# Kernel tuning notes

Hardware: AMD Instinct MI355X
Metric: run time of the kernel (lower is better)

## Reference

```python
import jax, jax.numpy as jnp
import numpy as np

B, C, T, N = 8, 128, 12, 4096
E_HALF = 131072
EPS = 1e-5


def _linear_params(key, fan_in, fan_out):
    kw, kb = jax.random.split(key)
    bound = 1.0 / np.sqrt(fan_in)
    W = jax.random.uniform(kw, (fan_in, fan_out), jnp.float32, -bound, bound)
    b = jax.random.uniform(kb, (fan_out,), jnp.float32, -bound, bound)
    return W, b


def setup_inputs() -> dict:
    key = jax.random.key(0)
    ks = jax.random.split(key, 10)
    h_in = jax.random.normal(ks[0], (B, C, T, N), jnp.float32)
    # symmetric edge list: random pairs + reverses + self loops
    u = jax.random.randint(ks[1], (E_HALF,), 0, N, jnp.int32)
    v = jax.random.randint(ks[2], (E_HALF,), 0, N, jnp.int32)
    loops = jnp.arange(N, dtype=jnp.int32)
    row = jnp.concatenate([u, v, loops])
    col = jnp.concatenate([v, u, loops])
    edge_index = jnp.stack([row, col])  # [2, E]
    Wq, bq = _linear_params(ks[3], C, C)
    Wk, bk = _linear_params(ks[4], C, C)
    Wv, bv = _linear_params(ks[5], C, C)
    W1, b1 = _linear_params(ks[6], 2 * C, 4 * C)
    W2, b2 = _linear_params(ks[7], 4 * C, C)
    W3, b3 = _linear_params(ks[8], C, 1)
    return dict(h_in=h_in, edge_index=edge_index, Wq=Wq, bq=bq, Wk=Wk, bk=bk,
                Wv=Wv, bv=bv, W1=W1, b1=b1, W2=W2, b2=b2, W3=W3, b3=b3)


def _masked_instance_norm(x, mask_f):
    # stats over the non-self-loop edges only (matching torch, where the MLP
    # only sees edge_index[:, non_self_loop_mask])
    cnt = mask_f.sum()
    mean = (x * mask_f).sum(0) / cnt
    var = (((x - mean) ** 2) * mask_f).sum(0) / cnt
    return (x - mean) / jnp.sqrt(var + EPS)


def _forward(h_in, edge_index, Wq, bq, Wk, bk, Wv, bv, W1, b1, W2, b2, W3, b3):
    # ---- TemporalAttention ----
    x = jnp.transpose(h_in, (0, 3, 2, 1))  # [B, N, T, C]
    q = x @ Wq + bq
    k = x @ Wk + bk
    v = x @ Wv + bv
    scores = jnp.einsum('bntc,bnsc->bnts', q, k) / (C ** 0.5)
    attn = jax.nn.softmax(scores, axis=-1)
    weighted = jnp.einsum('bnts,bnsc->bntc', attn, v)
    emb = weighted.sum(axis=2)          # [B, N, C]
    emb_mean = emb.mean(axis=0)         # [N, C]

    # ---- ExtractorMLP on non-self-loop edges ----
    row, col = edge_index[0], edge_index[1]
    self_loop = row == col
    mask_f = (~self_loop).astype(emb_mean.dtype)[:, None]  # [E, 1]
    f12 = jnp.concatenate([emb_mean[row], emb_mean[col]], axis=-1)  # [E, 2C]
    h = jax.nn.relu(_masked_instance_norm(f12 @ W1 + b1, mask_f))
    h = jax.nn.relu(_masked_instance_norm(h @ W2 + b2, mask_f))
    logits = h @ W3 + b3                 # [E, 1]

    # concrete_sample, eval mode (deterministic)
    att = jax.nn.sigmoid(logits)
    all_att = jnp.where(self_loop[:, None], 1.0, att)  # [E, 1]

    # ---- transpose + reorder_like: match each edge with its reverse ----
    M = jnp.max(edge_index) + 1
    fwd_key = row * M + col
    rev_key = col * M + row
    order = jnp.argsort(fwd_key)
    pos = jnp.searchsorted(fwd_key[order], rev_key)
    perm = order[pos]                    # index of reverse edge
    edge_att = (all_att + all_att[perm]) * 0.5
    return edge_att


def reference(h_in, edge_index, Wq, bq, Wk, bk, Wv, bv, W1, b1, W2, b2, W3, b3):
    return _forward(h_in, edge_index, Wq, bq, Wk, bk, Wv, bv, W1, b1, W2, b2, W3, b3)
```

## Files before the change

kernel.cpp:

```cpp
#include <hip/hip_runtime.h>
#include <hip/hip_bf16.h>

#define CC     128
#define TT     12
#define NNODE  4096
#define NE     266240
#define EHALF  131072
#define F1     512
#define EPS    1e-5f
#define RSQRTC 0.08838834764831845f
#define LOG2E  1.4426950408889634f
#define EBG    48
#define NBLKG2 5547
#define NF2B   87
#define ST     40

#define O_XWM   0ull
#define O_ICNT  524288ull
#define O_CNT   524416ull
#define O_T     528512ull
#define O_S     528640ull
#define O_T2    545024ull
#define O_GTB   561664ull
#define O_W0B   569856ull
#define O_WC1   569920ull
#define O_WC2   635456ull
#define O_B1C   700992ull
#define O_M1    701504ull
#define O_IS1   702016ull
#define O_M2    702528ull
#define O_AW    702656ull
#define O_W2T   702784ull
#define O_PB    735552ull
#define O_QB    1784128ull
#define O_ALLA  2832704ull
#define O_PART  3098944ull
#define O_PART2 4518976ull
#define O_Z2    4541248ull

typedef __attribute__((ext_vector_type(8))) short bf16x8;
typedef __attribute__((ext_vector_type(4))) float f32x4;

__device__ inline float bfbits2f(unsigned int v) { return __uint_as_float(v << 16); }
__device__ inline unsigned short f2bf(float x) {
  union { __hip_bfloat16 h; unsigned short u; } cv;
  cv.h = __float2bfloat16(x);
  return cv.u;
}
__device__ inline float f4get(const float4& v, int k) {
  return k == 0 ? v.x : k == 1 ? v.y : k == 2 ? v.z : v.w;
}

__global__ __launch_bounds__(256) void k_setup(
    const float* __restrict__ Wq, const float* __restrict__ bq,
    const float* __restrict__ Wk, const float* __restrict__ Wv,
    const float* __restrict__ bv, const float* __restrict__ W1,
    const float* __restrict__ b1, const float* __restrict__ W2,
    const int* __restrict__ row, const int* __restrict__ col,
    unsigned short* __restrict__ Gtb, unsigned short* __restrict__ w0b,
    float* __restrict__ Wc1, float* __restrict__ Wc2, float* __restrict__ b1c,
    unsigned short* __restrict__ W2T, int* __restrict__ cnt, int* __restrict__ icnt) {
  __shared__ float wvr[CC];
  __shared__ int h[NNODE];
  const int blk = blockIdx.x, tid = threadIdx.x;
  if (blk < 128) {
    if (tid < 128) {
      int i = blk, j = tid;
      float acc = 0.f;
      for (int co = 0; co < CC; ++co) acc = fmaf(Wq[i*CC+co], Wk[j*CC+co], acc);
      Gtb[j*CC + i] = f2bf(acc);
      if (j == 0) {
        float a = 0.f;
        for (int co = 0; co < CC; ++co) a = fmaf(Wk[i*CC+co], bq[co], a);
        w0b[i] = f2bf(a);
      }
    }
  } else if (blk < 256) {
    const int c = blk - 128;
    if (tid < CC) wvr[tid] = Wv[(size_t)c*CC + tid];
    __syncthreads();
    for (int hh = 0; hh < 2; ++hh) {
      int f = hh*256 + tid;
      float a1 = 0.f, a2 = 0.f;
      for (int j = 0; j < CC; ++j) {
        float wv = wvr[j];
        a1 = fmaf(wv, W1[(size_t)j*F1 + f], a1);
        a2 = fmaf(wv, W1[(size_t)(CC + j)*F1 + f], a2);
      }
      Wc1[(size_t)c*F1 + f] = a1;
      Wc2[(size_t)c*F1 + f] = a2;
    }
    if (c == 0) {
      for (int hh = 0; hh < 2; ++hh) {
        int f = hh*256 + tid;
        float s = b1[f];
        for (int j = 0; j < CC; ++j)
          s = fmaf(12.f*bv[j], W1[(size_t)j*F1 + f] + W1[(size_t)(CC + j)*F1 + f], s);
        b1c[f] = s;
      }
    }
  } else if (blk < 384) {
    const int n = blk - 256;
    for (int k = tid; k < F1; k += 256)
      W2T[(size_t)n*F1 + k] = f2bf(W2[(size_t)k*CC + n]);
  } else {
    for (int i = tid; i < NNODE; i += 256) h[i] = 0;
    __syncthreads();
    int lc = 0;
    const int base = (blk - 384) << 12;
    for (int i = tid; i < 4096; i += 256) {
      int e = base + i;
      int r = row[e], c = col[e];
      if (r != c) { atomicAdd(&h[r], 1); ++lc; }
    }
    #pragma unroll
    for (int d = 1; d < 64; d <<= 1) lc += __shfl_xor(lc, d);
    __syncthreads();
    for (int i = tid; i < NNODE; i += 256) { int v = h[i]; if (v) atomicAdd(&cnt[i], v); }
    if ((tid & 63) == 0) atomicAdd(icnt, lc);
  }
}

__global__ __launch_bounds__(256, 8) void k_attn(
    const float* __restrict__ h_in,
    const unsigned short* __restrict__ Gtb,
    const unsigned short* __restrict__ w0b,
    float* __restrict__ xwm) {
  __shared__ unsigned short xs[48*128];
  __shared__ unsigned short ys[49*128];
  const int tid = threadIdx.x;
  const int bid = ((blockIdx.x & 7) << 10) | (blockIdx.x >> 3);
  const int b  = bid >> 10;
  const int n0 = (bid & 1023) << 2;

  const int w = tid >> 6, lane = tid & 63;
  const int l15 = lane & 15, l4 = lane >> 4;

  {
    const int c2 = tid & 63;
    const float* g0 = h_in + (((size_t)b*CC + 2*c2)*TT + w)*NNODE + n0;
    float4 av[3], bv[3];
    #pragma unroll
    for (int it = 0; it < 3; ++it) {
      av[it] = *(const float4*)(g0 + (size_t)(4*it)*NNODE);
      bv[it] = *(const float4*)(g0 + (size_t)(TT + 4*it)*NNODE);
    }
    if (tid < 16) {
      uint4 wv = *(const uint4*)(w0b + (tid << 3));
      *(uint4*)((char*)ys + 48*256 + (tid << 4)) = wv;
    }
    #pragma unroll
    for (int it = 0; it < 3; ++it) {
      int t = w + it*4;
      #pragma unroll
      for (int i = 0; i < 4; ++i) {
        float xa = f4get(av[it], i);
        float xb = f4get(bv[it], i);
        int r = i*TT + t;
        unsigned byte = ((unsigned)r << 8) + (((unsigned)(c2*4)) ^ (((unsigned)(r & 7)) << 4));
        *(unsigned*)((char*)xs + byte) = (unsigned)f2bf(xa) | ((unsigned)f2bf(xb) << 16);
      }
    }
  }
  __syncthreads();

  {
    f32x4 acc[2][3];
    #pragma unroll
    for (int mt = 0; mt < 2; ++mt)
      #pragma unroll
      for (int nt = 0; nt < 3; ++nt) acc[mt][nt] = (f32x4){0.f,0.f,0.f,0.f};

    #pragma unroll
    for (int kt = 0; kt < 4; ++kt) {
      bf16x8 gf[2];
      #pragma unroll
      for (int mt = 0; mt < 2; ++mt)
        gf[mt] = *(const bf16x8*)(Gtb + (size_t)((w<<5) + (mt<<4) + l15)*CC + (kt<<5) + (l4<<3));
      bf16x8 bfr[3];
      #pragma unroll
      for (int nt = 0; nt < 3; ++nt) {
        int rr = nt*16 + l15;
        unsigned byte = ((unsigned)rr << 8) +
                        (((unsigned)((kt<<6) + (l4<<4))) ^ (((unsigned)(rr & 7)) << 4));
        bfr[nt] = *(const bf16x8*)((const char*)xs + byte);
      }
      #pragma unroll
      for (int mt = 0; mt < 2; ++mt)
        #pragma unroll
        for (int nt = 0; nt < 3; ++nt)
          acc[mt][nt] = __builtin_amdgcn_mfma_f32_16x16x32_bf16(gf[mt], bfr[nt], acc[mt][nt], 0, 0, 0);
    }
    #pragma unroll
    for (int mt = 0; mt < 2; ++mt)
      #pragma unroll
      for (int nt = 0; nt < 3; ++nt) {
        int rr = nt*16 + l15;
        ushort4 v;
        v.x = f2bf(acc[mt][nt][0]); v.y = f2bf(acc[mt][nt][1]);
        v.z = f2bf(acc[mt][nt][2]); v.w = f2bf(acc[mt][nt][3]);
        unsigned cb = (unsigned)((w<<6) + (mt<<5) + (l4<<3));
        unsigned byte = ((unsigned)rr << 8) + (cb ^ (((unsigned)(rr & 7)) << 4));
        *(ushort4*)((char*)ys + byte) = v;
      }
  }
  __syncthreads();

  {
    const int rb = w*TT;
    const bool sval = (l15 < TT);
    const int rr  = rb + (sval ? l15 : 0);
    const int rra = sval ? (rb + l15) : 48;
    f32x4 sa = (f32x4){0.f,0.f,0.f,0.f};
    #pragma unroll
    for (int kt = 0; kt < 4; ++kt) {
      unsigned kb = (unsigned)((kt<<6) + (l4<<4));
      unsigned byteA = ((unsigned)rra << 8) + (kb ^ (((unsigned)(rra & 7)) << 4));
      unsigned byteB = ((unsigned)rr  << 8) + (kb ^ (((unsigned)(rr  & 7)) << 4));
      bf16x8 afr = *(const bf16x8*)((const char*)ys + byteA);
      bf16x8 bfr = *(const bf16x8*)((const char*)xs + byteB);
      sa = __builtin_amdgcn_mfma_f32_16x16x32_bf16(afr, bfr, sa, 0, 0, 0);
    }
    float dv = __shfl(sa[0], 48 + l15);
    float p[4];
    #pragma unroll
    for (int r = 0; r < 4; ++r) {
      float t1 = sval ? (sa[r] + dv) * RSQRTC : -1e30f;
      float e = exp2f(t1 * LOG2E);
      float s = e;
      s += __shfl_xor(s, 1);
      s += __shfl_xor(s, 2);
      s += __shfl_xor(s, 4);
      s += __shfl_xor(s, 8);
      p[r] = e / s;
    }
    float wpart = (l4 < 3) ? (p[0] + p[1] + p[2] + p[3]) : 0.f;
    wpart += __shfl_xor(wpart, 16);
    wpart += __shfl_xor(wpart, 32);
    float xw0 = 0.f, xw1 = 0.f;
    #pragma unroll
    for (int s = 0; s < TT; ++s) {
      float wv = __shfl(wpart, s);
      int r2 = rb + s;
      unsigned byte = ((unsigned)r2 << 8) +
                      (((unsigned)(lane << 2)) ^ (((unsigned)(r2 & 7)) << 4));
      unsigned xp = *(const unsigned*)((const char*)xs + byte);
      xw0 = fmaf(wv, bfbits2f(xp & 0xffffu), xw0);
      xw1 = fmaf(wv, bfbits2f(xp >> 16), xw1);
    }
    unsafeAtomicAdd(&xwm[(size_t)(n0 + w)*CC + (lane << 1)],     xw0 * 0.125f);
    unsafeAtomicAdd(&xwm[(size_t)(n0 + w)*CC + (lane << 1) + 1], xw1 * 0.125f);
  }
}

__global__ __launch_bounds__(256) void k_ST2(const float* __restrict__ xwm,
    const int* __restrict__ row, const int* __restrict__ col,
    const int* __restrict__ cnt, float* __restrict__ S,
    float* __restrict__ T2, float* __restrict__ t) {
  __shared__ unsigned short XT[128*ST];
  __shared__ unsigned short YT[128*ST];
  __shared__ float tl[128];
  const int tid = threadIdx.x;
  const int w = tid >> 6, lane = tid & 63, l15 = lane & 15, l4 = lane >> 4;
  const int j = tid & 31, fi = tid >> 5;
  const int f0 = fi << 4;
  f32x4 acc[2][8];
  #pragma unroll
  for (int mt = 0; mt < 2; ++mt)
    #pragma unroll
    for (int nt = 0; nt < 8; ++nt) acc[mt][nt] = (f32x4){0.f,0.f,0.f,0.f};

  if (blockIdx.x < 512) {
    const int ebase = blockIdx.x << 9;
    for (int bt = 0; bt < 16; ++bt) {
      const int e = ebase + (bt << 5) + j;
      const int r = row[e], c = col[e];
      const bool msk = (r != c);
      const float* xr = xwm + (size_t)r*CC + f0;
      const float* xc = xwm + (size_t)c*CC + f0;
      float4 xv[4], yv[4];
      #pragma unroll
      for (int u = 0; u < 4; ++u) { xv[u] = *(const float4*)(xr + 4*u); yv[u] = *(const float4*)(xc + 4*u); }
      __syncthreads();
      #pragma unroll
      for (int u = 0; u < 16; ++u) {
        float xvv = f4get(xv[u >> 2], u & 3);
        float yvv = f4get(yv[u >> 2], u & 3);
        XT[(f0+u)*ST + j] = f2bf(xvv);
        YT[(f0+u)*ST + j] = msk ? f2bf(yvv) : (unsigned short)0;
      }
      __syncthreads();
      bf16x8 af[2];
      #pragma unroll
      for (int mt = 0; mt < 2; ++mt)
        af[mt] = *(const bf16x8*)&XT[((((w<<1)+mt)<<4) + l15)*ST + (l4<<3)];
      #pragma unroll
      for (int nt = 0; nt < 8; ++nt) {
        bf16x8 bf_ = *(const bf16x8*)&YT[(((nt<<4) + l15))*ST + (l4<<3)];
        acc[0][nt] = __builtin_amdgcn_mfma_f32_16x16x32_bf16(af[0], bf_, acc[0][nt], 0, 0, 0);
        acc[1][nt] = __builtin_amdgcn_mfma_f32_16x16x32_bf16(af[1], bf_, acc[1][nt], 0, 0, 0);
      }
    }
    #pragma unroll
    for (int mt = 0; mt < 2; ++mt)
      #pragma unroll
      for (int nt = 0; nt < 8; ++nt)
        #pragma unroll
        for (int reg = 0; reg < 4; ++reg) {
          int a = (((w<<1)+mt)<<4) + (l4<<2) + reg;
          int b = (nt<<4) + l15;
          unsafeAtomicAdd(&S[a*128 + b], acc[mt][nt][reg]);
        }
  } else {
    if (tid < 128) tl[tid] = 0.f;
    float tloc[16];
    #pragma unroll
    for (int u = 0; u < 16; ++u) tloc[u] = 0.f;
    const int nbase = (blockIdx.x - 512) << 7;
    for (int bt = 0; bt < 4; ++bt) {
      const int n = nbase + (bt << 5) + j;
      const float cw = (float)cnt[n];
      const float* xr = xwm + (size_t)n*CC + f0;
      float4 xv[4];
      #pragma unroll
      for (int u = 0; u < 4; ++u) xv[u] = *(const float4*)(xr + 4*u);
      __syncthreads();
      #pragma unroll
      for (int u = 0; u < 16; ++u) {
        float xvv = f4get(xv[u >> 2], u & 3);
        float yvv = cw * xvv;
        XT[(f0+u)*ST + j] = f2bf(xvv);
        YT[(f0+u)*ST + j] = f2bf(yvv);
        tloc[u] += yvv;
      }
      __syncthreads();
      bf16x8 af[2];
      #pragma unroll
      for (int mt = 0; mt < 2; ++mt)
        af[mt] = *(const bf16x8*)&XT[((((w<<1)+mt)<<4) + l15)*ST + (l4<<3)];
      #pragma unroll
      for (int nt = 0; nt < 8; ++nt) {
        bf16x8 bf_ = *(const bf16x8*)&YT[(((nt<<4) + l15))*ST + (l4<<3)];
        acc[0][nt] = __builtin_amdgcn_mfma_f32_16x16x32_bf16(af[0], bf_, acc[0][nt], 0, 0, 0);
        acc[1][nt] = __builtin_amdgcn_mfma_f32_16x16x32_bf16(af[1], bf_, acc[1][nt], 0, 0, 0);
      }
    }
    #pragma unroll
    for (int u = 0; u < 16; ++u) atomicAdd(&tl[f0 + u], tloc[u]);
    #pragma unroll
    for (int mt = 0; mt < 2; ++mt)
      #pragma unroll
      for (int nt = 0; nt < 8; ++nt)
        #pragma unroll
        for (int reg = 0; reg < 4; ++reg) {
          int a = (((w<<1)+mt)<<4) + (l4<<2) + reg;
          int b = (nt<<4) + l15;
          unsafeAtomicAdd(&T2[a*128 + b], acc[mt][nt][reg]);
        }
    __syncthreads();
    if (tid < 128) unsafeAtomicAdd(&t[tid], tl[tid]);
  }
}

__global__ __launch_bounds__(128) void k_stats(const float* __restrict__ S,
    const float* __restrict__ T2, const float* __restrict__ Wc1,
    const float* __restrict__ Wc2, const float* __restrict__ b1c,
    const float* __restrict__ t, const int* __restrict__ icnt,
    float* __restrict__ m1, float* __restrict__ is1) {
  __shared__ float w1c[128], w2c[128];
  __shared__ float redq[2], redt1[2], redt2[2];
  const int f = blockIdx.x, a = threadIdx.x;
  w1c[a] = Wc1[(size_t)a*F1 + f];
  w2c[a] = Wc2[(size_t)a*F1 + f];
  __syncthreads();
  float v1 = 0.f, v2 = 0.f, v3 = 0.f;
  const float* Sr = S + a*128;
  const float* Tr = T2 + a*128;
  for (int b = 0; b < 128; b += 4) {
    float4 sv = *(const float4*)(Sr + b);
    float4 tv = *(const float4*)(Tr + b);
    float4 w1v = *(const float4*)&w1c[b];
    float4 w2v = *(const float4*)&w2c[b];
    #pragma unroll
    for (int u = 0; u < 4; ++u) {
      v1 = fmaf(f4get(sv, u), f4get(w2v, u), v1);
      v2 = fmaf(f4get(tv, u), f4get(w1v, u), v2);
      v3 = fmaf(f4get(tv, u), f4get(w2v, u), v3);
    }
  }
  float pa  = w1c[a]*(v2 + 2.f*v1) + w2c[a]*v3;
  float ta1 = t[a]*w1c[a];
  float ta2 = t[a]*w2c[a];
  #pragma unroll
  for (int d = 1; d < 64; d <<= 1) {
    pa  += __shfl_xor(pa, d);
    ta1 += __shfl_xor(ta1, d);
    ta2 += __shfl_xor(ta2, d);
  }
  if ((a & 63) == 0) { redq[a>>6] = pa; redt1[a>>6] = ta1; redt2[a>>6] = ta2; }
  __syncthreads();
  if (a == 0) {
    float cntf = (float)(*icnt);
    float bb = b1c[f];
    float sumq = redq[0] + redq[1];
    float st1 = redt1[0] + redt1[1];
    float st2 = redt2[0] + redt2[1];
    float w2tot = sumq + 2.f*bb*(st1 + st2) + cntf*bb*bb;
    float w1tot = st1 + st2 + cntf*bb;
    float m = w1tot / cntf;
    m1[f] = m;
    is1[f] = rsqrtf(w2tot/cntf - m*m + EPS);
  }
}

__global__ __launch_bounds__(256) void k_pq(const float* __restrict__ xwm,
    const float* __restrict__ Wc1, const float* __restrict__ Wc2,
    const float* __restrict__ b1c, const float* __restrict__ m1,
    const float* __restrict__ is1,
    unsigned short* __restrict__ Pb, unsigned short* __restrict__ Qb) {
  __shared__ float em[4][CC];
  const int tid = threadIdx.x;
  const int n0 = blockIdx.x << 2;
  for (int i = tid; i < 4*CC; i += 256)
    em[i >> 7][i & 127] = xwm[(size_t)(n0 + (i >> 7))*CC + (i & 127)];
  __syncthreads();
  for (int half = 0; half < 2; ++half) {
    const int f = half*256 + tid;
    const float mm = m1[f], ii = is1[f], bb = b1c[f];
    for (int nn = 0; nn < 4; ++nn) {
      float ap = bb, aq = 0.f;
      for (int c = 0; c < CC; ++c) {
        float e = em[nn][c];
        ap = fmaf(e, Wc1[(size_t)c*F1 + f], ap);
        aq = fmaf(e, Wc2[(size_t)c*F1 + f], aq);
      }
      Pb[(size_t)(n0+nn)*F1 + f] = f2bf(ap * ii);
      Qb[(size_t)(n0+nn)*F1 + f] = f2bf((aq - mm) * ii);
    }
  }
}

__global__ __launch_bounds__(512, 6) void k_gemm(const unsigned short* __restrict__ Pb,
    const unsigned short* __restrict__ Qb, const int* __restrict__ row,
    const int* __restrict__ col,
    const unsigned short* __restrict__ W2T, const float* __restrict__ b2,
    unsigned short* __restrict__ z2, float* __restrict__ part) {
  __shared__ unsigned short h1s[EBG*F1];
  __shared__ int rS[EBG], cS[EBG]; __shared__ float mk[EBG];
  __shared__ float cstat[256];
  const int tid = threadIdx.x;
  const int bid = blockIdx.x;
  const int e0 = bid * EBG;
  const int w = tid >> 6, lane = tid & 63;
  const int wn0 = w << 4;
  const int l15 = lane & 15, l4 = lane >> 4;
  if (tid < EBG) {
    int e = e0 + tid;
    bool valid = e < NE;
    int r = valid ? row[e] : 0, c = valid ? col[e] : 0;
    rS[tid] = r; cS[tid] = c; mk[tid] = (valid && r != c) ? 1.f : 0.f;
  }
  __syncthreads();

  #pragma unroll
  for (int rr = 0; rr < 2; ++rr) {
    int jj[3], cc[3];
    #pragma unroll
    for (int s = 0; s < 3; ++s) {
      int i = tid + ((rr*3 + s) << 9);
      jj[s] = i >> 6; cc[s] = i & 63;
    }
    uint4 pv[3], qv[3];
    #pragma unroll
    for (int s = 0; s < 3; ++s) pv[s] = *(const uint4*)(Pb + (size_t)rS[jj[s]]*F1 + (cc[s] << 3));
    #pragma unroll
    for (int s = 0; s < 3; ++s) qv[s] = *(const uint4*)(Qb + (size_t)cS[jj[s]]*F1 + (cc[s] << 3));
    #pragma unroll
    for (int s = 0; s < 3; ++s) {
      unsigned out[4];
      #pragma unroll
      for (int q = 0; q < 4; ++q) {
        unsigned pu = (&pv[s].x)[q], qu = (&qv[s].x)[q];
        float ha = fmaxf(bfbits2f(pu & 0xffffu) + bfbits2f(qu & 0xffffu), 0.f);
        float hb = fmaxf(bfbits2f(pu >> 16)     + bfbits2f(qu >> 16),     0.f);
        out[q] = (unsigned)f2bf(ha) | ((unsigned)f2bf(hb) << 16);
      }
      unsigned byte = ((unsigned)jj[s] << 10) +
                      (((unsigned)(cc[s] << 4)) ^ (((unsigned)(jj[s] & 7)) << 4));
      *(uint4*)((char*)h1s + byte) = make_uint4(out[0], out[1], out[2], out[3]);
    }
  }
  __syncthreads();

  f32x4 acc[3];
  #pragma unroll
  for (int a = 0; a < 3; ++a) acc[a] = (f32x4){0.f,0.f,0.f,0.f};

  const unsigned short* w2p = W2T + (size_t)(wn0 + l15)*F1 + (l4 << 3);
  #pragma unroll
  for (int kt = 0; kt < 16; ++kt) {
    bf16x8 bfr = *(const bf16x8*)(w2p + (kt << 5));
    bf16x8 afr[3];
    #pragma unroll
    for (int mt = 0; mt < 3; ++mt) {
      int j = (mt << 4) + l15;
      unsigned byte = ((unsigned)j << 10) + (((unsigned)(kt*64 + l4*16)) ^ ((j & 7) << 4));
      afr[mt] = *(const bf16x8*)((const char*)h1s + byte);
    }
    #pragma unroll
    for (int mt = 0; mt < 3; ++mt)
      acc[mt] = __builtin_amdgcn_mfma_f32_16x16x32_bf16(afr[mt], bfr, acc[mt], 0, 0, 0);
  }
  __syncthreads();

  float* z2s = (float*)&h1s[0];
  const int colg = wn0 + l15;
  {
    float bb = b2[colg];
    float sloc = 0.f, qloc = 0.f;
    #pragma unroll
    for (int mt = 0; mt < 3; ++mt) {
      f32x4 v = acc[mt];
      #pragma unroll
      for (int reg = 0; reg < 4; ++reg) {
        int j = (mt << 4) + (l4 << 2) + reg;
        float z = v[reg] + bb;
        float m = mk[j];
        sloc = fmaf(m, z, sloc);
        qloc = fmaf(m*z, z, qloc);
        z2s[j*132 + colg] = z;
      }
    }
    sloc += __shfl_xor(sloc, 16); sloc += __shfl_xor(sloc, 32);
    qloc += __shfl_xor(qloc, 16); qloc += __shfl_xor(qloc, 32);
    if (l4 == 0) { cstat[colg] = sloc; cstat[128 + colg] = qloc; }
  }
  __syncthreads();

  #pragma unroll
  for (int p = 0; p < 2; ++p) {
    int idx = (p << 12) + (tid << 3);
    if (idx < EBG*CC) {
      int j = idx >> 7, c = idx & 127;
      if (e0 + j < NE) {
        const float* src = &z2s[j*132 + c];
        float4 v0 = *(const float4*)src;
        float4 v1 = *(const float4*)(src + 4);
        uint4 o;
        o.x = (unsigned)f2bf(v0.x) | ((unsigned)f2bf(v0.y) << 16);
        o.y = (unsigned)f2bf(v0.z) | ((unsigned)f2bf(v0.w) << 16);
        o.z = (unsigned)f2bf(v1.x) | ((unsigned)f2bf(v1.y) << 16);
        o.w = (unsigned)f2bf(v1.z) | ((unsigned)f2bf(v1.w) << 16);
        *(uint4*)(z2 + (size_t)e0*CC + idx) = o;
      }
    }
  }
  if (tid < 256) part[(size_t)bid*256 + tid] = cstat[tid];
}

__global__ __launch_bounds__(256) void k_fin2a(const float* __restrict__ part,
                                               float* __restrict__ part2) {
  const int g = blockIdx.x, tid = threadIdx.x;
  float s = 0.f;
  for (int r = 0; r < 64; ++r) {
    int b = g*64 + r;
    if (b < NBLKG2) s += part[(size_t)b*256 + tid];
  }
  part2[(size_t)g*256 + tid] = s;
}

__global__ __launch_bounds__(256) void k_fin2b(const float* __restrict__ part2,
    const int* __restrict__ icnt, const float* __restrict__ W3,
    float* __restrict__ m2, float* __restrict__ aw) {
  __shared__ float red[256];
  const int tid = threadIdx.x;
  float s = 0.f;
  for (int g = 0; g < NF2B; ++g) s += part2[(size_t)g*256 + tid];
  red[tid] = s;
  __syncthreads();
  if (tid < 128) {
    float cnt = (float)(*icnt);
    float m = red[tid] / cnt;
    m2[tid] = m;
    aw[tid] = rsqrtf(red[128 + tid]/cnt - m*m + EPS) * W3[tid];
  }
}

__global__ __launch_bounds__(256) void k_score(const unsigned short* __restrict__ z2,
    const int* __restrict__ row, const int* __restrict__ col,
    const float* __restrict__ m2, const float* __restrict__ aw,
    const float* __restrict__ b3, float* __restrict__ all_att) {
  const int tid = threadIdx.x;
  const int w = tid >> 6, lane = tid & 63;
  const int g = lane >> 4, sub = lane & 15;
  const int f0 = sub << 3;
  float mv[8], av[8];
  {
    float4 a0 = *(const float4*)(m2 + f0);
    float4 a1 = *(const float4*)(m2 + f0 + 4);
    float4 b0 = *(const float4*)(aw + f0);
    float4 b1 = *(const float4*)(aw + f0 + 4);
    #pragma unroll
    for (int u = 0; u < 4; ++u) { mv[u] = f4get(a0, u); mv[4+u] = f4get(a1, u); }
    #pragma unroll
    for (int u = 0; u < 4; ++u) { av[u] = f4get(b0, u); av[4+u] = f4get(b1, u); }
  }
  const float bb = b3[0];
  #pragma unroll
  for (int it = 0; it < 4; ++it) {
    const int e = (blockIdx.x << 6) + (w << 4) + (it << 2) + g;
    uint4 zv = *(const uint4*)(z2 + (size_t)e*CC + f0);
    float a = 0.f;
    #pragma unroll
    for (int u = 0; u < 4; ++u) {
      unsigned zu = (&zv.x)[u];
      float z0 = bfbits2f(zu & 0xffffu);
      float z1 = bfbits2f(zu >> 16);
      a += (z0 > mv[2*u])   ? (z0 - mv[2*u])*av[2*u]     : 0.f;
      a += (z1 > mv[2*u+1]) ? (z1 - mv[2*u+1])*av[2*u+1] : 0.f;
    }
    a += __shfl_xor(a, 1);
    a += __shfl_xor(a, 2);
    a += __shfl_xor(a, 4);
    a += __shfl_xor(a, 8);
    if (sub == 0) {
      int r = row[e], c = col[e];
      all_att[e] = (r == c) ? 1.f : 1.f/(1.f + expf(-(a + bb)));
    }
  }
}

__global__ __launch_bounds__(256) void k_out(const float* __restrict__ all_att,
    float* __restrict__ out) {
  int e = blockIdx.x*256 + threadIdx.x;
  int p = (e < EHALF) ? (e + EHALF) : (e < 2*EHALF ? e - EHALF : e);
  out[e] = 0.5f * (all_att[e] + all_att[p]);
}

extern "C" void kernel_launch(void* const* d_in, const int* in_sizes, int n_in,
                              void* d_out, int out_size, void* d_ws, size_t ws_size,
                              hipStream_t stream) {
  const float* h_in = (const float*)d_in[0];
  const int*   ei   = (const int*)d_in[1];
  const float* Wq = (const float*)d_in[2];
  const float* bq = (const float*)d_in[3];
  const float* Wk = (const float*)d_in[4];
  const float* bk = (const float*)d_in[5];  (void)bk;
  const float* Wv = (const float*)d_in[6];
  const float* bv = (const float*)d_in[7];
  const float* W1 = (const float*)d_in[8];
  const float* b1 = (const float*)d_in[9];
  const float* W2 = (const float*)d_in[10];
  const float* b2 = (const float*)d_in[11];
  const float* W3 = (const float*)d_in[12];
  const float* b3 = (const float*)d_in[13];
  float* ws = (float*)d_ws;
  float* out = (float*)d_out;
  const int* row = ei;
  const int* col = ei + NE;

  hipMemsetAsync(ws, 0, 561664ull * 4ull, stream);

  k_setup<<<448, 256, 0, stream>>>(Wq, bq, Wk, Wv, bv, W1, b1, W2, row, col,
                                   (unsigned short*)(ws+O_GTB), (unsigned short*)(ws+O_W0B),
                                   ws+O_WC1, ws+O_WC2, ws+O_B1C,
                                   (unsigned short*)(ws+O_W2T),
                                   (int*)(ws+O_CNT), (int*)(ws+O_ICNT));
  k_attn<<<8192, 256, 0, stream>>>(h_in, (const unsigned short*)(ws+O_GTB),
                                   (const unsigned short*)(ws+O_W0B), ws+O_XWM);
  k_ST2<<<544, 256, 0, stream>>>(ws+O_XWM, row, col, (const int*)(ws+O_CNT),
                                 ws+O_S, ws+O_T2, ws+O_T);
  k_stats<<<512, 128, 0, stream>>>(ws+O_S, ws+O_T2, ws+O_WC1, ws+O_WC2, ws+O_B1C,
                                   ws+O_T, (const int*)(ws+O_ICNT), ws+O_M1, ws+O_IS1);
  k_pq<<<1024, 256, 0, stream>>>(ws+O_XWM, ws+O_WC1, ws+O_WC2, ws+O_B1C,
                                 ws+O_M1, ws+O_IS1,
                                 (unsigned short*)(ws+O_PB), (unsigned short*)(ws+O_QB));
  k_gemm<<<NBLKG2, 512, 0, stream>>>((const unsigned short*)(ws+O_PB),
                                     (const unsigned short*)(ws+O_QB), row, col,
                                     (const unsigned short*)(ws+O_W2T), b2,
                                     (unsigned short*)(ws+O_Z2), ws+O_PART);
  k_fin2a<<<NF2B, 256, 0, stream>>>(ws+O_PART, ws+O_PART2);
  k_fin2b<<<1, 256, 0, stream>>>(ws+O_PART2, (const int*)(ws+O_ICNT), W3,
                                 ws+O_M2, ws+O_AW);
  k_score<<<4160, 256, 0, stream>>>((const unsigned short*)(ws+O_Z2), row, col,
                                    ws+O_M2, ws+O_AW, b3, ws+O_ALLA);
  k_out<<<1040, 256, 0, stream>>>(ws+O_ALLA, out);
}
```

Baseline: 425.1 us.

## Process eight nodes per attention block with 512 threads

The attention kernel now handles 8 nodes per block with 512 threads instead of 4 nodes with 256, doubling the shared-memory tiles and splitting waves into an M-group and a node-group for the projection GEMM. The load mapping changes to 32-byte contiguous node segments per (channel, time) row, and the block-to-(batch,node) mapping is no longer swizzled. The intent is to reuse Gtb fragment loads across more nodes, improve global-load granularity and cut block count. In exchange it uses more LDS per block, which can lower occupancy.

```diff
diff --git a/kernel.cpp b/kernel.cpp
--- a/kernel.cpp
+++ b/kernel.cpp
@@ -121,50 +121,48 @@
   }
 }
 
-__global__ __launch_bounds__(256, 8) void k_attn(
+__global__ __launch_bounds__(512, 6) void k_attn(
     const float* __restrict__ h_in,
     const unsigned short* __restrict__ Gtb,
     const unsigned short* __restrict__ w0b,
     float* __restrict__ xwm) {
-  __shared__ unsigned short xs[48*128];
-  __shared__ unsigned short ys[49*128];
+  __shared__ unsigned short xs[96*128];
+  __shared__ unsigned short ys[97*128];
   const int tid = threadIdx.x;
-  const int bid = ((blockIdx.x & 7) << 10) | (blockIdx.x >> 3);
-  const int b  = bid >> 10;
-  const int n0 = (bid & 1023) << 2;
+  const int b  = blockIdx.x & 7;
+  const int n0 = (blockIdx.x >> 3) << 3;
 
   const int w = tid >> 6, lane = tid & 63;
   const int l15 = lane & 15, l4 = lane >> 4;
 
   {
-    const int c2 = tid & 63;
-    const float* g0 = h_in + (((size_t)b*CC + 2*c2)*TT + w)*NNODE + n0;
-    float4 av[3], bv[3];
-    #pragma unroll
-    for (int it = 0; it < 3; ++it) {
-      av[it] = *(const float4*)(g0 + (size_t)(4*it)*NNODE);
-      bv[it] = *(const float4*)(g0 + (size_t)(TT + 4*it)*NNODE);
-    }
     if (tid < 16) {
       uint4 wv = *(const uint4*)(w0b + (tid << 3));
-      *(uint4*)((char*)ys + 48*256 + (tid << 4)) = wv;
-    }
-    #pragma unroll
-    for (int it = 0; it < 3; ++it) {
-      int t = w + it*4;
+      *(uint4*)((char*)ys + 96*256 + (tid << 4)) = wv;
+    }
+    #pragma unroll
+    for (int k = 0; k < 3; ++k) {
+      int p = tid + (k << 9);
+      int half = p & 1;
+      int q = p >> 1;
+      int t = q % 12;
+      int c2 = q / 12;
+      const float* g = h_in + (((size_t)b*CC + 2*c2)*TT + t)*NNODE + n0 + half*4;
+      float4 a0 = *(const float4*)g;
+      float4 a1 = *(const float4*)(g + (size_t)TT*NNODE);
       #pragma unroll
       for (int i = 0; i < 4; ++i) {
-        float xa = f4get(av[it], i);
-        float xb = f4get(bv[it], i);
-        int r = i*TT + t;
+        int r = (half*4 + i)*TT + t;
         unsigned byte = ((unsigned)r << 8) + (((unsigned)(c2*4)) ^ (((unsigned)(r & 7)) << 4));
-        *(unsigned*)((char*)xs + byte) = (unsigned)f2bf(xa) | ((unsigned)f2bf(xb) << 16);
+        *(unsigned*)((char*)xs + byte) = (unsigned)f2bf(f4get(a0, i)) |
+                                         ((unsigned)f2bf(f4get(a1, i)) << 16);
       }
     }
   }
   __syncthreads();
 
   {
+    const int wm = w & 3, wg = w >> 2;
     f32x4 acc[2][3];
     #pragma unroll
     for (int mt = 0; mt < 2; ++mt)
@@ -176,11 +174,11 @@
       bf16x8 gf[2];
       #pragma unroll
       for (int mt = 0; mt < 2; ++mt)
-        gf[mt] = *(const bf16x8*)(Gtb + (size_t)((w<<5) + (mt<<4) + l15)*CC + (kt<<5) + (l4<<3));
+        gf[mt] = *(const bf16x8*)(Gtb + (size_t)((wm<<5) + (mt<<4) + l15)*CC + (kt<<5) + (l4<<3));
       bf16x8 bfr[3];
       #pragma unroll
       for (int nt = 0; nt < 3; ++nt) {
-        int rr = nt*16 + l15;
+        int rr = wg*48 + nt*16 + l15;
         unsigned byte = ((unsigned)rr << 8) +
                         (((unsigned)((kt<<6) + (l4<<4))) ^ (((unsigned)(rr & 7)) << 4));
         bfr[nt] = *(const bf16x8*)((const char*)xs + byte);
@@ -195,11 +193,11 @@
     for (int mt = 0; mt < 2; ++mt)
       #pragma unroll
       for (int nt = 0; nt < 3; ++nt) {
-        int rr = nt*16 + l15;
+        int rr = wg*48 + nt*16 + l15;
         ushort4 v;
         v.x = f2bf(acc[mt][nt][0]); v.y = f2bf(acc[mt][nt][1]);
         v.z = f2bf(acc[mt][nt][2]); v.w = f2bf(acc[mt][nt][3]);
-        unsigned cb = (unsigned)((w<<6) + (mt<<5) + (l4<<3));
+        unsigned cb = (unsigned)((wm<<6) + (mt<<5) + (l4<<3));
         unsigned byte = ((unsigned)rr << 8) + (cb ^ (((unsigned)(rr & 7)) << 4));
         *(ushort4*)((char*)ys + byte) = v;
       }
@@ -210,7 +208,7 @@
     const int rb = w*TT;
     const bool sval = (l15 < TT);
     const int rr  = rb + (sval ? l15 : 0);
-    const int rra = sval ? (rb + l15) : 48;
+    const int rra = sval ? (rb + l15) : 96;
     f32x4 sa = (f32x4){0.f,0.f,0.f,0.f};
     #pragma unroll
     for (int kt = 0; kt < 4; ++kt) {
@@ -666,7 +664,7 @@
                                    ws+O_WC1, ws+O_WC2, ws+O_B1C,
                                    (unsigned short*)(ws+O_W2T),
                                    (int*)(ws+O_CNT), (int*)(ws+O_ICNT));
-  k_attn<<<8192, 256, 0, stream>>>(h_in, (const unsigned short*)(ws+O_GTB),
+  k_attn<<<4096, 512, 0, stream>>>(h_in, (const unsigned short*)(ws+O_GTB),
                                    (const unsigned short*)(ws+O_W0B), ws+O_XWM);
   k_ST2<<<544, 256, 0, stream>>>(ws+O_XWM, row, col, (const int*)(ws+O_CNT),
                                  ws+O_S, ws+O_T2, ws+O_T);
```

New measurement: 408.6 us. 1.04x faster.
